# Performance work log

Measured on AMD Instinct MI355X. Metric: run time of the kernel, lower is better.

Reference implementation:

```python
import jax, jax.numpy as jnp
import numpy as np

HEAD_DIM = 128
N_HEADS = 32
ROPE_DIM = 64
TOPK = 1024
B, S, HID, QLORA = 1, 2048, 4096, 1536
LN_EPS = 1e-5  # torch nn.LayerNorm default


def _hadamard_matrix(n):
    H = np.array([[1.0]], dtype=np.float32)
    while H.shape[0] < n:
        H = np.block([[H, H], [H, -H]])
    return jnp.asarray(H)

_H128 = _hadamard_matrix(HEAD_DIM)
_FWHT_SCALE = HEAD_DIM ** -0.5


def rotate_activation(x):
    # Fast Walsh-Hadamard transform == x @ H_sylvester, scaled by dim**-0.5
    return (x @ _H128) * _FWHT_SCALE


def rope_non_interleaved(x, cos, sin):
    # x: [..., rope_dim]; cos/sin: broadcastable [..., rope_dim/2]
    half = x.shape[-1] // 2
    x1, x2 = x[..., :half], x[..., half:]
    return jnp.concatenate([x1 * cos - x2 * sin, x1 * sin + x2 * cos], axis=-1)


def setup_inputs() -> dict:
    key = jax.random.key(0)
    ks = jax.random.split(key, 8)
    hidden_states = jax.random.normal(ks[0], (B, S, HID), jnp.float32)
    q_compressed = jax.random.normal(ks[1], (B, S, QLORA), jnp.float32)
    # rotary cos/sin for rope_dim=64 (standard concat layout)
    pos = jnp.arange(S, dtype=jnp.float32)
    inv_freq = 1.0 / (10000.0 ** (jnp.arange(0, ROPE_DIM, 2, dtype=jnp.float32) / ROPE_DIM))
    ang = pos[:, None] * inv_freq[None, :]  # [S, 32]
    cos = jnp.tile(jnp.cos(ang), (1, 2))[None]  # [1, S, 64]
    sin = jnp.tile(jnp.sin(ang), (1, 2))[None]
    # additive causal mask [B, S, S]
    causal = jnp.tril(jnp.ones((S, S), jnp.bool_))
    attention_mask = jnp.where(causal, 0.0, -1e9).astype(jnp.float32)[None]
    Wq_b = jax.random.normal(ks[2], (QLORA, N_HEADS * HEAD_DIM), jnp.float32) * (QLORA ** -0.5)
    Wk = jax.random.normal(ks[3], (HID, HEAD_DIM), jnp.float32) * (HID ** -0.5)
    k_gamma = jnp.ones((HEAD_DIM,), jnp.float32)
    k_beta = jnp.zeros((HEAD_DIM,), jnp.float32)
    Ww = jax.random.normal(ks[4], (HID, N_HEADS), jnp.float32) * (HID ** -0.5)
    return {"hidden_states": hidden_states, "q_compressed": q_compressed, "cos": cos,
            "sin": sin, "attention_mask": attention_mask, "Wq_b": Wq_b, "Wk": Wk,
            "k_gamma": k_gamma, "k_beta": k_beta, "Ww": Ww}


def reference(hidden_states, q_compressed, cos, sin, attention_mask, Wq_b, Wk, k_gamma, k_beta, Ww):
    b, s, _ = hidden_states.shape
    softmax_scale = HEAD_DIM ** -0.5
    # queries: [b, s, H, D]
    q = (q_compressed @ Wq_b).reshape(b, s, N_HEADS, HEAD_DIM)
    q_rope, q_nope = q[..., :ROPE_DIM], q[..., ROPE_DIM:]
    # keys: single shared head, LayerNorm(k)
    k = hidden_states @ Wk  # [b, s, D]
    mu = jnp.mean(k, axis=-1, keepdims=True)
    var = jnp.mean(jnp.square(k - mu), axis=-1, keepdims=True)
    k = (k - mu) * jax.lax.rsqrt(var + LN_EPS) * k_gamma + k_beta
    k_rope, k_nope = k[..., :ROPE_DIM], k[..., ROPE_DIM:]
    # non-interleaved RoPE (cos/sin truncated to half_dim=32)
    half = ROPE_DIM // 2
    c, sn = cos[..., :half], sin[..., :half]
    q_rope = rope_non_interleaved(q_rope, c[:, :, None, :], sn[:, :, None, :])
    k_rope = rope_non_interleaved(k_rope, c, sn)
    q = jnp.concatenate([q_rope, q_nope], axis=-1)
    k = jnp.concatenate([k_rope, k_nope], axis=-1)
    # Hadamard activation rotation
    q = rotate_activation(q)
    k = rotate_activation(k)
    # I_{t,s} = sum_h w_{t,h} * ReLU(q_{t,h} . k_s) * scale
    scores = jax.nn.relu(jnp.einsum('bthd,bsd->bths', q, k)) * softmax_scale
    weights = hidden_states @ Ww  # [b, t, H]
    index_scores = jnp.einsum('bths,bth->bts', scores, weights)
    index_scores = index_scores + attention_mask
    topk = min(TOPK, s)
    _, topk_indices = jax.lax.top_k(index_scores, topk)  # [b, s, topk]
    return topk_indices, index_scores
```

## Files before the change

kernel.cpp:

```cpp
#include <hip/hip_runtime.h>
#include <stdint.h>

#define S_LEN 2048
#define HID 4096
#define QLORA 1536
#define NH 32
#define HD 128
#define TOPK_N 1024
#define NEG_INF -1000000000.0f
#define INV_SQRT_HD 0.08838834764831844f

typedef __attribute__((ext_vector_type(8))) short short8;
typedef __attribute__((ext_vector_type(4))) short short4_;
typedef __attribute__((ext_vector_type(4))) float float4_;
typedef __attribute__((ext_vector_type(4))) unsigned uint4_;
typedef __attribute__((ext_vector_type(4))) int int4_;
typedef __attribute__((ext_vector_type(2))) int int2_;

__device__ __forceinline__ short f2bf(float x) {
  union { float f; unsigned u; } v; v.f = x;
  unsigned r = v.u + 0x7FFFu + ((v.u >> 16) & 1u);
  return (short)(r >> 16);
}

__device__ __forceinline__ unsigned f2ord(float x) {
  union { float f; unsigned u; } v; v.f = x;
  return v.u ^ (0x80000000u | (unsigned)((int)v.u >> 31));
}

__device__ __forceinline__ void gload_lds16(const void* g, void* l) {
  __builtin_amdgcn_global_load_lds((const __attribute__((address_space(1))) unsigned int*)g,
                                   (__attribute__((address_space(3))) unsigned int*)l, 16, 0, 0);
}

__global__ __launch_bounds__(256) void prep_kernel(
    const float* __restrict__ hidden, short* __restrict__ hidb,
    const float* __restrict__ qc, char* __restrict__ qc8,
    float* __restrict__ kacc,
    const float* __restrict__ wqb, char* __restrict__ wq8T,
    const float* __restrict__ wk, const float* __restrict__ ww,
    short* __restrict__ kwT) {
  __shared__ __align__(8) char stile[4352];
  int bid = blockIdx.x;
  const int tid = threadIdx.x;
  if (bid < 8192) {
    int i = bid * 256 + tid;
    float4 v = ((const float4*)hidden)[i];
    short4_ o;
    o[0] = f2bf(v.x); o[1] = f2bf(v.y); o[2] = f2bf(v.z); o[3] = f2bf(v.w);
    ((short4_*)hidb)[i] = o;
    return;
  }
  if (bid < 9728) {
    int i = (bid - 8192) * 256 + tid;
    float4 f0 = ((const float4*)qc)[i * 2];
    float4 f1 = ((const float4*)qc)[i * 2 + 1];
    int lo = 0, hi = 0;
    lo = __builtin_amdgcn_cvt_pk_fp8_f32(f0.x, f0.y, lo, 0);
    lo = __builtin_amdgcn_cvt_pk_fp8_f32(f0.z, f0.w, lo, 1);
    hi = __builtin_amdgcn_cvt_pk_fp8_f32(f1.x, f1.y, hi, 0);
    hi = __builtin_amdgcn_cvt_pk_fp8_f32(f1.z, f1.w, hi, 1);
    ((int2_*)qc8)[i] = (int2_){lo, hi};
    return;
  }
  if (bid < 10048) {
    int i = (bid - 9728) * 256 + tid;
    ((float4_*)kacc)[i] = (float4_){0.f, 0.f, 0.f, 0.f};
    return;
  }
  if (bid < 13120) {
    char (*t8)[33] = (char(*)[33])stile;
    int b = bid - 10048;
    int k0 = (b >> 7) * 64, n0 = (b & 127) * 32;
    #pragma unroll
    for (int i = 0; i < 8; i++) {
      int e = tid + i * 256;
      int r = e >> 5, c = e & 31;
      float x = wqb[(size_t)(k0 + r) * HID + n0 + c];
      t8[r][c] = (char)__builtin_amdgcn_cvt_pk_fp8_f32(x, x, 0, 0);
    }
    __syncthreads();
    int nl = tid >> 3, jk = (tid & 7) * 8;
    union { char c[8]; long l; } o;
    #pragma unroll
    for (int j = 0; j < 8; j++) o.c[j] = t8[jk + j][nl];
    *(long*)(wq8T + (size_t)(n0 + nl) * QLORA + k0 + jk) = o.l;
    return;
  }
  short (*tile)[33] = (short(*)[33])stile;
  const float* in; short* out; int R, C, bx, by;
  if (bid < 13632) {
    int b2 = bid - 13120;
    in = wk; out = kwT; R = HID; C = HD; bx = b2 & 3; by = b2 >> 2;
  } else {
    int b3 = bid - 13632;
    in = ww; out = kwT + 128 * HID; R = HID; C = NH; bx = 0; by = b3;
  }
  int c0 = bx * 32, r0 = by * 32;
  int tx = tid & 31, ty = tid >> 5;
  #pragma unroll
  for (int i = 0; i < 32; i += 8)
    tile[ty + i][tx] = f2bf(in[(size_t)(r0 + ty + i) * C + c0 + tx]);
  __syncthreads();
  #pragma unroll
  for (int i = 0; i < 32; i += 8)
    out[(size_t)(c0 + ty + i) * R + r0 + tx] = tile[tx][ty + i];
}

#define QSTAGE8(kt, Ad, Bd) do { \
  _Pragma("unroll") \
  for (int i = 0; i < 4; i++) { \
    int m = w * 32 + i * 8 + lr; \
    int gb = (kt) * 128 + ((lc ^ (m & 7)) << 4); \
    gload_lds16(qc8 + (size_t)(t0 + m) * QLORA + gb, (Ad) + (w * 32 + i * 8) * 128); \
    gload_lds16(wq8T + (size_t)(n0 + m) * QLORA + gb, (Bd) + (w * 32 + i * 8) * 128); \
  } \
} while (0)

#define QCOMPUTE8(Aq, Bq) do { \
  _Pragma("unroll") \
  for (int p = 0; p < 4; p++) { \
    int ch = p * 2 + (quad >> 1); \
    int lo8 = (quad & 1) * 8; \
    long a[2], b[8]; \
    _Pragma("unroll") \
    for (int mt = 0; mt < 2; mt++) { \
      int m = w * 32 + mt * 16 + l15; \
      a[mt] = *(const long*)((Aq) + m * 128 + ((ch ^ (m & 7)) << 4) + lo8); \
    } \
    _Pragma("unroll") \
    for (int nt = 0; nt < 8; nt++) { \
      int n = nt * 16 + l15; \
      b[nt] = *(const long*)((Bq) + n * 128 + ((ch ^ (n & 7)) << 4) + lo8); \
    } \
    _Pragma("unroll") \
    for (int mt = 0; mt < 2; mt++) \
      _Pragma("unroll") \
      for (int nt = 0; nt < 8; nt++) \
        acc[mt][nt] = __builtin_amdgcn_mfma_f32_16x16x32_fp8_fp8(a[mt], b[nt], acc[mt][nt], 0, 0, 0); \
  } \
} while (0)

__global__ __launch_bounds__(256, 4) void gemms_kernel(
    const char* __restrict__ qc8, const char* __restrict__ wq8T,
    const float* __restrict__ cosp, const float* __restrict__ sinp,
    short* __restrict__ qrot,
    const short* __restrict__ hidb, const short* __restrict__ kwT,
    float* __restrict__ kacc) {
  __shared__ __align__(16) char smem[32768];
  const int tid = threadIdx.x;
  const int w = tid >> 6, lane = tid & 63;
  const int l15 = lane & 15, quad = lane >> 4;
  const int lr = lane >> 3, lc = lane & 7;

  if (blockIdx.x < 512) {
    char* A0 = smem;
    char* B0 = smem + 16384;
    const int n0 = (blockIdx.x & 31) * 128;
    const int t0 = (blockIdx.x >> 5) * 128;

    float4_ acc[2][8];
    #pragma unroll
    for (int mt = 0; mt < 2; mt++)
      #pragma unroll
      for (int i = 0; i < 8; i++) acc[mt][i] = (float4_){0.f, 0.f, 0.f, 0.f};

    QSTAGE8(0, A0, B0);
    __syncthreads();
    for (int kt = 0; ; kt++) {
      QCOMPUTE8(A0, B0);
      if (kt == 11) break;
      __syncthreads();
      QSTAGE8(kt + 1, A0, B0);
      __syncthreads();
    }

    #pragma unroll
    for (int mt = 0; mt < 2; mt++) {
      #pragma unroll
      for (int r = 0; r < 4; r++) {
        const int trow = t0 + w * 32 + mt * 16 + quad * 4 + r;
        float v[8];
        #pragma unroll
        for (int nt = 0; nt < 8; nt++) v[nt] = acc[mt][nt][r];
        float cc0 = cosp[trow * 64 + l15], cc1 = cosp[trow * 64 + 16 + l15];
        float ss0 = sinp[trow * 64 + l15], ss1 = sinp[trow * 64 + 16 + l15];
        float r0 = v[0] * cc0 - v[2] * ss0, r1 = v[1] * cc1 - v[3] * ss1;
        float r2 = v[0] * ss0 + v[2] * cc0, r3 = v[1] * ss1 + v[3] * cc1;
        v[0] = r0; v[1] = r1; v[2] = r2; v[3] = r3;
        short* orow = qrot + (size_t)trow * HID + n0;
        #pragma unroll
        for (int nt = 0; nt < 8; nt++)
          orow[nt * 16 + l15] = f2bf(v[nt]);
      }
    }
  } else {
    short* Al = (short*)smem;
    short* Bl = (short*)(smem + 8192);
    const int b2 = blockIdx.x - 512;
    const int kc0 = (b2 & 7) * 512;
    const int m0g = (b2 >> 3) * 64;

    float4_ acc[10];
    #pragma unroll
    for (int i = 0; i < 10; i++) acc[i] = (float4_){0.f, 0.f, 0.f, 0.f};

    for (int k0 = kc0; k0 < kc0 + 512; k0 += 64) {
      #pragma unroll
      for (int i = 0; i < 2; i++) {
        int m = w * 16 + i * 8 + lr;
        int gk = k0 + ((lc ^ (m & 7)) << 3);
        gload_lds16(hidb + (size_t)(m0g + m) * HID + gk, Al + (w * 16 + i * 8) * 64);
      }
      #pragma unroll
      for (int i = 0; i < 5; i++) {
        int n = w * 40 + i * 8 + lr;
        int gk = k0 + ((lc ^ (n & 7)) << 3);
        gload_lds16(kwT + (size_t)n * HID + gk, Bl + (w * 40 + i * 8) * 64);
      }
      __syncthreads();
      #pragma unroll
      for (int kk = 0; kk < 64; kk += 32) {
        int ca = (kk >> 3) + quad;
        int ma = w * 16 + l15;
        short8 a = *(const short8*)(Al + ma * 64 + ((ca ^ (ma & 7)) << 3));
        #pragma unroll
        for (int nt = 0; nt < 10; nt++) {
          int n = nt * 16 + l15;
          short8 b = *(const short8*)(Bl + n * 64 + ((ca ^ (n & 7)) << 3));
          acc[nt] = __builtin_amdgcn_mfma_f32_16x16x32_bf16(a, b, acc[nt], 0, 0, 0);
        }
      }
      __syncthreads();
    }
    #pragma unroll
    for (int nt = 0; nt < 10; nt++)
      #pragma unroll
      for (int r = 0; r < 4; r++) {
        int row = m0g + w * 16 + quad * 4 + r;
        atomicAdd(&kacc[(size_t)row * 160 + nt * 16 + l15], acc[nt][r]);
      }
  }
}

__global__ __launch_bounds__(256) void ln_rope_kernel(
    const float* __restrict__ kacc, const float* __restrict__ gamma,
    const float* __restrict__ beta, const float* __restrict__ cosp,
    const float* __restrict__ sinp, short* __restrict__ krot) {
  const int tid = threadIdx.x;
  const int row = blockIdx.x * 16 + (tid >> 4);
  const int l16 = tid & 15;
  const int c0 = l16 * 8;
  const float* rp = kacc + (size_t)row * 160 + c0;
  float4 f0 = ((const float4*)rp)[0], f1 = ((const float4*)rp)[1];
  float v[8] = {f0.x, f0.y, f0.z, f0.w, f1.x, f1.y, f1.z, f1.w};
  float s = 0.f, ss = 0.f;
  #pragma unroll
  for (int j = 0; j < 8; j++) { s += v[j]; ss += v[j] * v[j]; }
  #pragma unroll
  for (int d = 1; d <= 8; d <<= 1) {
    s += __shfl_xor(s, d, 64); ss += __shfl_xor(ss, d, 64);
  }
  float mu = s * (1.0f / 128.0f);
  float var = ss * (1.0f / 128.0f) - mu * mu;
  float rs = rsqrtf(var + 1e-5f);
  #pragma unroll
  for (int j = 0; j < 8; j++)
    v[j] = (v[j] - mu) * rs * gamma[c0 + j] + beta[c0 + j];
  #pragma unroll
  for (int j = 0; j < 8; j++) {
    float p = __shfl_xor(v[j], 4, 64);
    if (l16 < 8) {
      int idx = (c0 + j) & 31;
      float c = cosp[row * 64 + idx], sn = sinp[row * 64 + idx];
      v[j] = v[j] * c + p * ((l16 < 4) ? -sn : sn);
    }
  }
  short8 o;
  #pragma unroll
  for (int j = 0; j < 8; j++) o[j] = f2bf(v[j]);
  *(short8*)(krot + (size_t)row * 128 + c0) = o;
}

__global__ __launch_bounds__(256, 4) void scores_kernel(
    const short* __restrict__ qrot, const short* __restrict__ krot,
    const float* __restrict__ kacc, float* __restrict__ isc) {
  __shared__ __align__(16) char smem[32768];
  short* buf0 = (short*)smem;
  short* buf1 = (short*)(smem + 16384);

  const int tid = threadIdx.x;
  const int w = tid >> 6, lane = tid & 63;
  const int l15 = lane & 15, quad = lane >> 4;
  const int wm = w >> 1, wn = w & 1;
  const int lr16 = lane >> 4, lc16 = lane & 15;

  const int bid = blockIdx.x;
  const int strip = (bid & 1) ? (1023 - (bid >> 1)) : (bid >> 1);
  const int t0 = strip * 2;
  const int nch = (t0 + 1) / 64 + 1;

  const short* Abase = qrot + (size_t)t0 * 32 * 128;
  #pragma unroll
  for (int i = 0; i < 4; i++) {
    int m = (w * 4 + i) * 4 + lr16;
    int gofs = m * 128 + ((lc16 ^ (m & 7)) << 3);
    gload_lds16(Abase + gofs, buf1 + (w * 4 + i) * 512);
    gload_lds16(krot + gofs, buf0 + (w * 4 + i) * 512);
  }
  __syncthreads();

  short8 af[4][2];
  #pragma unroll
  for (int k4 = 0; k4 < 4; k4++) {
    int ca = k4 * 4 + quad;
    #pragma unroll
    for (int mt = 0; mt < 2; mt++) {
      int m = wm * 32 + mt * 16 + l15;
      af[k4][mt] = *(const short8*)(buf1 + m * 128 + ((ca ^ (m & 7)) << 3));
    }
  }
  const int trow = t0 + wm;
  float wq[2][4];
  #pragma unroll
  for (int mt = 0; mt < 2; mt++)
    #pragma unroll
    for (int r = 0; r < 4; r++)
      wq[mt][r] = kacc[(size_t)trow * 160 + 128 + mt * 16 + quad * 4 + r];
  __syncthreads();

  int cur = 0;
  for (int c = 0; c < nch; c++) {
    short* bcur = cur ? buf1 : buf0;
    if (c + 1 < nch) {
      short* bnxt = cur ? buf0 : buf1;
      const short* Bbase = krot + (size_t)(c + 1) * 64 * 128;
      #pragma unroll
      for (int i = 0; i < 4; i++) {
        int m = (w * 4 + i) * 4 + lr16;
        int gofs = m * 128 + ((lc16 ^ (m & 7)) << 3);
        gload_lds16(Bbase + gofs, bnxt + (w * 4 + i) * 512);
      }
    }

    float4_ acc[2][2];
    #pragma unroll
    for (int mt = 0; mt < 2; mt++)
      #pragma unroll
      for (int nt = 0; nt < 2; nt++) acc[mt][nt] = (float4_){0.f, 0.f, 0.f, 0.f};

    #pragma unroll
    for (int k4 = 0; k4 < 4; k4++) {
      int ca = k4 * 4 + quad;
      short8 b[2];
      #pragma unroll
      for (int nt = 0; nt < 2; nt++) {
        int n = wn * 32 + nt * 16 + l15;
        b[nt] = *(const short8*)(bcur + n * 128 + ((ca ^ (n & 7)) << 3));
      }
      #pragma unroll
      for (int mt = 0; mt < 2; mt++)
        #pragma unroll
        for (int nt = 0; nt < 2; nt++)
          acc[mt][nt] = __builtin_amdgcn_mfma_f32_16x16x32_bf16(af[k4][mt], b[nt], acc[mt][nt], 0, 0, 0);
    }

    #pragma unroll
    for (int nt = 0; nt < 2; nt++) {
      float p = 0.f;
      #pragma unroll
      for (int r = 0; r < 4; r++)
        p += fmaxf(acc[0][nt][r], 0.f) * wq[0][r] + fmaxf(acc[1][nt][r], 0.f) * wq[1][r];
      p += __shfl_xor(p, 16, 64); p += __shfl_xor(p, 32, 64);
      int s = c * 64 + wn * 32 + nt * 16 + l15;
      if (quad == 0)
        isc[(size_t)trow * S_LEN + s] = (s <= trow) ? p * INV_SQRT_HD : NEG_INF;
    }

    __syncthreads();
    cur ^= 1;
  }

  if (w < 2) {
    float4_ nf = (float4_){NEG_INF, NEG_INF, NEG_INF, NEG_INF};
    float4_* rowp = (float4_*)(isc + (size_t)(t0 + w) * S_LEN);
    for (int i = nch * 16 + lane; i < 512; i += 64) rowp[i] = nf;
  }
}


__device__ __forceinline__ void ce(unsigned &a, unsigned &b, bool d) {
  unsigned mx = a > b ? a : b;
  unsigned mn = a > b ? b : a;
  a = d ? mx : mn;
  b = d ? mn : mx;
}

__device__ __forceinline__ void mtop3(unsigned* v, bool d) {
  #pragma unroll
  for (int j = 16; j >= 4; j >>= 1)
    #pragma unroll
    for (int r = 0; r < 32; ++r)
      if (!(r & j)) ce(v[r], v[r ^ j], d);
}

template <int JT>
__device__ __forceinline__ void mreg(unsigned* v, bool d) {
  #pragma unroll
  for (int j = JT; j >= 1; j >>= 1)
    #pragma unroll
    for (int r = 0; r < 32; ++r)
      if (!(r & j)) ce(v[r], v[r ^ j], d);
}

#define IDX_L0   ((l << 5) | (q << 2))
#define IDX_654  (((l >> 2) << 7) | (q << 4) | ((l & 3) << 2))
#define IDX_765  (((l >> 3) << 8) | (q << 5) | ((l & 7) << 2))
#define IDX_876  (((l >> 4) << 9) | (q << 6) | ((l & 15) << 2))
#define IDX_543  (((l >> 1) << 6) | (q << 3) | ((l & 1) << 2))
#define IDX_987  (((l >> 5) << 10) | (q << 7) | ((l & 31) << 2))
#define IDX_1098 ((q << 8) | (l << 2))
#define SWZW(ix) ((ix) ^ ((((ix) >> 5) & 7) << 2))

#define RT(FROM, TO) do {                                               \
  _Pragma("unroll")                                                     \
  for (int q = 0; q < 8; ++q) {                                         \
    int ix = (FROM);                                                    \
    *(uint4_*)(buf + SWZW(ix)) =                                        \
        (uint4_){v[4 * q], v[4 * q + 1], v[4 * q + 2], v[4 * q + 3]};   \
  }                                                                     \
  _Pragma("unroll")                                                     \
  for (int q = 0; q < 8; ++q) {                                         \
    int ix = (TO);                                                      \
    uint4_ u = *(const uint4_*)(buf + SWZW(ix));                        \
    v[4 * q] = u[0]; v[4 * q + 1] = u[1];                               \
    v[4 * q + 2] = u[2]; v[4 * q + 3] = u[3];                           \
  }                                                                     \
} while (0)

__global__ __launch_bounds__(256) void topk_kernel(const float* __restrict__ isc,
                                                   int* __restrict__ idx_out) {
  __shared__ __align__(16) unsigned sbuf[4][2048];
  const int tid = threadIdx.x;
  const int w = tid >> 6, l = tid & 63;
  unsigned* buf = sbuf[w];
  const int gid = blockIdx.x * 4 + w;
  const bool shortrow = (gid < 512);
  int trow, sbase;
  if (shortrow) { trow = gid * 2 + (l >> 5); sbase = (l & 31) << 5; }
  else          { trow = 512 + gid;          sbase = l << 5; }

  unsigned v[32];
  {
    const float* rp = isc + (size_t)trow * S_LEN + sbase;
    #pragma unroll
    for (int g = 0; g < 8; ++g) {
      float4 f = ((const float4*)rp)[g];
      unsigned b0 = (unsigned)(2047 - (sbase + g * 4));
      v[g * 4 + 0] = (f2ord(f.x) & 0xFFFFF800u) | b0;
      v[g * 4 + 1] = (f2ord(f.y) & 0xFFFFF800u) | (b0 - 1);
      v[g * 4 + 2] = (f2ord(f.z) & 0xFFFFF800u) | (b0 - 2);
      v[g * 4 + 3] = (f2ord(f.w) & 0xFFFFF800u) | (b0 - 3);
    }
  }

  #pragma unroll
  for (int r = 0; r < 32; r += 2) ce(v[r], v[r + 1], ((r & 2) == 0));
  #pragma unroll
  for (int j = 2; j >= 1; j >>= 1)
    #pragma unroll
    for (int r = 0; r < 32; ++r)
      if (!(r & j)) ce(v[r], v[r ^ j], ((r & 4) == 0));
  #pragma unroll
  for (int j = 4; j >= 1; j >>= 1)
    #pragma unroll
    for (int r = 0; r < 32; ++r)
      if (!(r & j)) ce(v[r], v[r ^ j], ((r & 8) == 0));
  #pragma unroll
  for (int j = 8; j >= 1; j >>= 1)
    #pragma unroll
    for (int r = 0; r < 32; ++r)
      if (!(r & j)) ce(v[r], v[r ^ j], ((r & 16) == 0));

  mreg<16>(v, (l & 1) == 0);

  {
    bool d = ((l & 2) == 0);
    bool keep = (((l & 1) == 0) == d);
    #pragma unroll
    for (int r = 0; r < 32; ++r) {
      unsigned pv = (unsigned)__shfl_xor((int)v[r], 1, 64);
      unsigned mx = v[r] > pv ? v[r] : pv;
      unsigned mn = v[r] > pv ? pv : v[r];
      v[r] = keep ? mx : mn;
    }
    mreg<16>(v, d);
  }

  {
    bool d = ((l & 4) == 0);
    RT(IDX_L0, IDX_654);  mtop3(v, d);
    RT(IDX_654, IDX_L0);  mreg<8>(v, d);
  }
  {
    bool d = ((l & 8) == 0);
    RT(IDX_L0, IDX_765);  mtop3(v, d);
    RT(IDX_765, IDX_L0);  mreg<16>(v, d);
  }
  {
    bool d = ((l & 16) == 0);
    RT(IDX_L0, IDX_876);  mtop3(v, d);
    RT(IDX_876, IDX_543); mtop3(v, d);
    RT(IDX_543, IDX_L0);  mreg<4>(v, d);
  }
  {
    bool d = shortrow ? true : (l < 32);
    RT(IDX_L0, IDX_987);  mtop3(v, d);
    RT(IDX_987, IDX_654); mtop3(v, d);
    RT(IDX_654, IDX_L0);  mreg<8>(v, d);
  }
  if (!shortrow) {
    RT(IDX_L0, IDX_1098); mtop3(v, true);
    RT(IDX_1098, IDX_765); mtop3(v, true);
    RT(IDX_765, IDX_L0);  mreg<16>(v, true);
  }

  if (shortrow || l < 32) {
    int* op = idx_out + (size_t)trow * TOPK_N + sbase;
    #pragma unroll
    for (int g = 0; g < 8; ++g) {
      int4_ o;
      #pragma unroll
      for (int j = 0; j < 4; ++j) o[j] = 2047 - (int)(v[g * 4 + j] & 0x7FFu);
      ((int4_*)op)[g] = o;
    }
  }
}

extern "C" void kernel_launch(void* const* d_in, const int* in_sizes, int n_in,
                              void* d_out, int out_size, void* d_ws, size_t ws_size,
                              hipStream_t stream) {
  const float* hidden = (const float*)d_in[0];
  const float* qc     = (const float*)d_in[1];
  const float* cosp   = (const float*)d_in[2];
  const float* sinp   = (const float*)d_in[3];
  const float* wqb    = (const float*)d_in[5];
  const float* wk     = (const float*)d_in[6];
  const float* gamma  = (const float*)d_in[7];
  const float* beta   = (const float*)d_in[8];
  const float* ww     = (const float*)d_in[9];

  char* ws = (char*)d_ws;
  short* hidb = (short*)ws;
  char*  qc8  = (char*)(ws + 16777216);
  char*  wq8T = (char*)(ws + 19922944);
  short* kwT  = (short*)(ws + 26214400);
  short* krot = (short*)(ws + 27525120);
  short* qrot = (short*)(ws + 28049408);
  float* kacc = (float*)(ws + 44826624);

  int*   idx_out = (int*)d_out;
  float* isc     = ((float*)d_out) + (size_t)S_LEN * TOPK_N;

  prep_kernel<<<dim3(13760), dim3(256), 0, stream>>>(hidden, hidb, qc, qc8, kacc,
                                                     wqb, wq8T, wk, ww, kwT);
  gemms_kernel<<<dim3(768), dim3(256), 0, stream>>>(qc8, wq8T, cosp, sinp, qrot,
                                                    hidb, kwT, kacc);
  ln_rope_kernel<<<dim3(128), dim3(256), 0, stream>>>(kacc, gamma, beta, cosp, sinp, krot);
  scores_kernel<<<dim3(1024), dim3(256), 0, stream>>>(qrot, krot, kacc, isc);
  topk_kernel<<<dim3(384), dim3(256), 0, stream>>>(isc, idx_out);
}
```

Measured before the change: 226.3 us.

## Restructure scores kernel to one row per block with direct global register loads

The scores kernel now processes one query row per block over 2048 blocks instead of two rows per block, with each of four waves covering 16 keys per 64-key chunk. LDS staging and block barriers are dropped: A and B fragments are loaded straight from global memory into registers, with a two-chunk software double buffer in registers. This cuts synchronisation and LDS traffic and gives finer load balance across the causal triangle. In exchange each key row is fetched once per query row rather than being shared between two rows, so L2 traffic rises and the loads are uncoalesced.

New measurement: 259.6 us. 1.15x slower.

```diff
diff --git a/kernel.cpp b/kernel.cpp
--- a/kernel.cpp
+++ b/kernel.cpp
@@ -282,110 +282,70 @@
   *(short8*)(krot + (size_t)row * 128 + c0) = o;
 }
 
+#define SLOADB(bf, c) do {                                                     \
+  const short* Bb = krot + (size_t)((c) * 64 + w * 16 + l15) * 128 + quad * 8; \
+  bf[0] = *(const short8*)(Bb);                                                \
+  bf[1] = *(const short8*)(Bb + 32);                                           \
+  bf[2] = *(const short8*)(Bb + 64);                                           \
+  bf[3] = *(const short8*)(Bb + 96);                                           \
+} while (0)
+
+#define SCSTORE(bf, c) do {                                                    \
+  float4_ a0 = (float4_){0.f, 0.f, 0.f, 0.f};                                  \
+  float4_ a1 = (float4_){0.f, 0.f, 0.f, 0.f};                                  \
+  _Pragma("unroll")                                                            \
+  for (int k4 = 0; k4 < 4; k4++) {                                             \
+    a0 = __builtin_amdgcn_mfma_f32_16x16x32_bf16(af[k4][0], bf[k4], a0, 0, 0, 0); \
+    a1 = __builtin_amdgcn_mfma_f32_16x16x32_bf16(af[k4][1], bf[k4], a1, 0, 0, 0); \
+  }                                                                            \
+  float p = 0.f;                                                               \
+  _Pragma("unroll")                                                            \
+  for (int r = 0; r < 4; r++)                                                  \
+    p += fmaxf(a0[r], 0.f) * wq[0][r] + fmaxf(a1[r], 0.f) * wq[1][r];          \
+  p += __shfl_xor(p, 16, 64); p += __shfl_xor(p, 32, 64);                      \
+  int s = (c) * 64 + w * 16 + l15;                                             \
+  if (quad == 0)                                                               \
+    isc[(size_t)trow * S_LEN + s] = (s <= trow) ? p * INV_SQRT_HD : NEG_INF;   \
+} while (0)
+
 __global__ __launch_bounds__(256, 4) void scores_kernel(
     const short* __restrict__ qrot, const short* __restrict__ krot,
     const float* __restrict__ kacc, float* __restrict__ isc) {
-  __shared__ __align__(16) char smem[32768];
-  short* buf0 = (short*)smem;
-  short* buf1 = (short*)(smem + 16384);
-
   const int tid = threadIdx.x;
   const int w = tid >> 6, lane = tid & 63;
   const int l15 = lane & 15, quad = lane >> 4;
-  const int wm = w >> 1, wn = w & 1;
-  const int lr16 = lane >> 4, lc16 = lane & 15;
-
-  const int bid = blockIdx.x;
-  const int strip = (bid & 1) ? (1023 - (bid >> 1)) : (bid >> 1);
-  const int t0 = strip * 2;
-  const int nch = (t0 + 1) / 64 + 1;
-
-  const short* Abase = qrot + (size_t)t0 * 32 * 128;
-  #pragma unroll
-  for (int i = 0; i < 4; i++) {
-    int m = (w * 4 + i) * 4 + lr16;
-    int gofs = m * 128 + ((lc16 ^ (m & 7)) << 3);
-    gload_lds16(Abase + gofs, buf1 + (w * 4 + i) * 512);
-    gload_lds16(krot + gofs, buf0 + (w * 4 + i) * 512);
-  }
-  __syncthreads();
+
+  const int trow = 2047 - blockIdx.x;
+  const int nch = (trow + 64) >> 6;
 
   short8 af[4][2];
-  #pragma unroll
-  for (int k4 = 0; k4 < 4; k4++) {
-    int ca = k4 * 4 + quad;
-    #pragma unroll
-    for (int mt = 0; mt < 2; mt++) {
-      int m = wm * 32 + mt * 16 + l15;
-      af[k4][mt] = *(const short8*)(buf1 + m * 128 + ((ca ^ (m & 7)) << 3));
-    }
-  }
-  const int trow = t0 + wm;
+  const short* Ab = qrot + (size_t)trow * HID + quad * 8;
+  #pragma unroll
+  for (int k4 = 0; k4 < 4; k4++)
+    #pragma unroll
+    for (int mt = 0; mt < 2; mt++)
+      af[k4][mt] = *(const short8*)(Ab + (mt * 16 + l15) * 128 + k4 * 32);
+
   float wq[2][4];
   #pragma unroll
   for (int mt = 0; mt < 2; mt++)
     #pragma unroll
     for (int r = 0; r < 4; r++)
       wq[mt][r] = kacc[(size_t)trow * 160 + 128 + mt * 16 + quad * 4 + r];
-  __syncthreads();
-
-  int cur = 0;
-  for (int c = 0; c < nch; c++) {
-    short* bcur = cur ? buf1 : buf0;
-    if (c + 1 < nch) {
-      short* bnxt = cur ? buf0 : buf1;
-      const short* Bbase = krot + (size_t)(c + 1) * 64 * 128;
-      #pragma unroll
-      for (int i = 0; i < 4; i++) {
-        int m = (w * 4 + i) * 4 + lr16;
-        int gofs = m * 128 + ((lc16 ^ (m & 7)) << 3);
-        gload_lds16(Bbase + gofs, bnxt + (w * 4 + i) * 512);
-      }
-    }
-
-    float4_ acc[2][2];
-    #pragma unroll
-    for (int mt = 0; mt < 2; mt++)
-      #pragma unroll
-      for (int nt = 0; nt < 2; nt++) acc[mt][nt] = (float4_){0.f, 0.f, 0.f, 0.f};
-
-    #pragma unroll
-    for (int k4 = 0; k4 < 4; k4++) {
-      int ca = k4 * 4 + quad;
-      short8 b[2];
-      #pragma unroll
-      for (int nt = 0; nt < 2; nt++) {
-        int n = wn * 32 + nt * 16 + l15;
-        b[nt] = *(const short8*)(bcur + n * 128 + ((ca ^ (n & 7)) << 3));
-      }
-      #pragma unroll
-      for (int mt = 0; mt < 2; mt++)
-        #pragma unroll
-        for (int nt = 0; nt < 2; nt++)
-          acc[mt][nt] = __builtin_amdgcn_mfma_f32_16x16x32_bf16(af[k4][mt], b[nt], acc[mt][nt], 0, 0, 0);
-    }
-
-    #pragma unroll
-    for (int nt = 0; nt < 2; nt++) {
-      float p = 0.f;
-      #pragma unroll
-      for (int r = 0; r < 4; r++)
-        p += fmaxf(acc[0][nt][r], 0.f) * wq[0][r] + fmaxf(acc[1][nt][r], 0.f) * wq[1][r];
-      p += __shfl_xor(p, 16, 64); p += __shfl_xor(p, 32, 64);
-      int s = c * 64 + wn * 32 + nt * 16 + l15;
-      if (quad == 0)
-        isc[(size_t)trow * S_LEN + s] = (s <= trow) ? p * INV_SQRT_HD : NEG_INF;
-    }
-
-    __syncthreads();
-    cur ^= 1;
-  }
-
-  if (w < 2) {
-    float4_ nf = (float4_){NEG_INF, NEG_INF, NEG_INF, NEG_INF};
-    float4_* rowp = (float4_*)(isc + (size_t)(t0 + w) * S_LEN);
-    for (int i = nch * 16 + lane; i < 512; i += 64) rowp[i] = nf;
-  }
+
+  short8 bA[4], bB[4];
+  SLOADB(bA, 0);
+  for (int c = 0; c < nch; c += 2) {
+    if (c + 1 < nch) SLOADB(bB, c + 1);
+    SCSTORE(bA, c);
+    if (c + 1 >= nch) break;
+    if (c + 2 < nch) SLOADB(bA, c + 2);
+    SCSTORE(bB, c + 1);
+  }
+
+  float4_ nf = (float4_){NEG_INF, NEG_INF, NEG_INF, NEG_INF};
+  float4_* rowp = (float4_*)(isc + (size_t)trow * S_LEN);
+  for (int i = nch * 16 + tid; i < 512; i += 256) rowp[i] = nf;
 }
 
 
@@ -567,6 +527,6 @@
   gemms_kernel<<<dim3(768), dim3(256), 0, stream>>>(qc8, wq8T, cosp, sinp, qrot,
                                                     hidb, kwT, kacc);
   ln_rope_kernel<<<dim3(128), dim3(256), 0, stream>>>(kacc, gamma, beta, cosp, sinp, krot);
-  scores_kernel<<<dim3(1024), dim3(256), 0, stream>>>(qrot, krot, kacc, isc);
+  scores_kernel<<<dim3(2048), dim3(256), 0, stream>>>(qrot, krot, kacc, isc);
   topk_kernel<<<dim3(384), dim3(256), 0, stream>>>(isc, idx_out);
 }
```

## Fuse scores and top-k into one kernel using LDS row buffer

Applied to the files above, without the earlier changes.

Merges the scores kernel and the bitonic top-k kernel. Each block now keeps its two score rows in shared memory and sorts them itself, so the top-k pass no longer reloads the rows from global memory and one launch is removed. The cost is more LDS per block (48KB), lower occupancy (launch bound 3), and only two of the four waves working during the sort. Short rows now go through the full 2048-element sort instead of the cheaper half-row path.

New measurement: 239.5 us. 1.06x slower.

```diff
diff --git a/kernel.cpp b/kernel.cpp
--- a/kernel.cpp
+++ b/kernel.cpp
@@ -282,113 +282,6 @@
   *(short8*)(krot + (size_t)row * 128 + c0) = o;
 }
 
-__global__ __launch_bounds__(256, 4) void scores_kernel(
-    const short* __restrict__ qrot, const short* __restrict__ krot,
-    const float* __restrict__ kacc, float* __restrict__ isc) {
-  __shared__ __align__(16) char smem[32768];
-  short* buf0 = (short*)smem;
-  short* buf1 = (short*)(smem + 16384);
-
-  const int tid = threadIdx.x;
-  const int w = tid >> 6, lane = tid & 63;
-  const int l15 = lane & 15, quad = lane >> 4;
-  const int wm = w >> 1, wn = w & 1;
-  const int lr16 = lane >> 4, lc16 = lane & 15;
-
-  const int bid = blockIdx.x;
-  const int strip = (bid & 1) ? (1023 - (bid >> 1)) : (bid >> 1);
-  const int t0 = strip * 2;
-  const int nch = (t0 + 1) / 64 + 1;
-
-  const short* Abase = qrot + (size_t)t0 * 32 * 128;
-  #pragma unroll
-  for (int i = 0; i < 4; i++) {
-    int m = (w * 4 + i) * 4 + lr16;
-    int gofs = m * 128 + ((lc16 ^ (m & 7)) << 3);
-    gload_lds16(Abase + gofs, buf1 + (w * 4 + i) * 512);
-    gload_lds16(krot + gofs, buf0 + (w * 4 + i) * 512);
-  }
-  __syncthreads();
-
-  short8 af[4][2];
-  #pragma unroll
-  for (int k4 = 0; k4 < 4; k4++) {
-    int ca = k4 * 4 + quad;
-    #pragma unroll
-    for (int mt = 0; mt < 2; mt++) {
-      int m = wm * 32 + mt * 16 + l15;
-      af[k4][mt] = *(const short8*)(buf1 + m * 128 + ((ca ^ (m & 7)) << 3));
-    }
-  }
-  const int trow = t0 + wm;
-  float wq[2][4];
-  #pragma unroll
-  for (int mt = 0; mt < 2; mt++)
-    #pragma unroll
-    for (int r = 0; r < 4; r++)
-      wq[mt][r] = kacc[(size_t)trow * 160 + 128 + mt * 16 + quad * 4 + r];
-  __syncthreads();
-
-  int cur = 0;
-  for (int c = 0; c < nch; c++) {
-    short* bcur = cur ? buf1 : buf0;
-    if (c + 1 < nch) {
-      short* bnxt = cur ? buf0 : buf1;
-      const short* Bbase = krot + (size_t)(c + 1) * 64 * 128;
-      #pragma unroll
-      for (int i = 0; i < 4; i++) {
-        int m = (w * 4 + i) * 4 + lr16;
-        int gofs = m * 128 + ((lc16 ^ (m & 7)) << 3);
-        gload_lds16(Bbase + gofs, bnxt + (w * 4 + i) * 512);
-      }
-    }
-
-    float4_ acc[2][2];
-    #pragma unroll
-    for (int mt = 0; mt < 2; mt++)
-      #pragma unroll
-      for (int nt = 0; nt < 2; nt++) acc[mt][nt] = (float4_){0.f, 0.f, 0.f, 0.f};
-
-    #pragma unroll
-    for (int k4 = 0; k4 < 4; k4++) {
-      int ca = k4 * 4 + quad;
-      short8 b[2];
-      #pragma unroll
-      for (int nt = 0; nt < 2; nt++) {
-        int n = wn * 32 + nt * 16 + l15;
-        b[nt] = *(const short8*)(bcur + n * 128 + ((ca ^ (n & 7)) << 3));
-      }
-      #pragma unroll
-      for (int mt = 0; mt < 2; mt++)
-        #pragma unroll
-        for (int nt = 0; nt < 2; nt++)
-          acc[mt][nt] = __builtin_amdgcn_mfma_f32_16x16x32_bf16(af[k4][mt], b[nt], acc[mt][nt], 0, 0, 0);
-    }
-
-    #pragma unroll
-    for (int nt = 0; nt < 2; nt++) {
-      float p = 0.f;
-      #pragma unroll
-      for (int r = 0; r < 4; r++)
-        p += fmaxf(acc[0][nt][r], 0.f) * wq[0][r] + fmaxf(acc[1][nt][r], 0.f) * wq[1][r];
-      p += __shfl_xor(p, 16, 64); p += __shfl_xor(p, 32, 64);
-      int s = c * 64 + wn * 32 + nt * 16 + l15;
-      if (quad == 0)
-        isc[(size_t)trow * S_LEN + s] = (s <= trow) ? p * INV_SQRT_HD : NEG_INF;
-    }
-
-    __syncthreads();
-    cur ^= 1;
-  }
-
-  if (w < 2) {
-    float4_ nf = (float4_){NEG_INF, NEG_INF, NEG_INF, NEG_INF};
-    float4_* rowp = (float4_*)(isc + (size_t)(t0 + w) * S_LEN);
-    for (int i = nch * 16 + lane; i < 512; i += 64) rowp[i] = nf;
-  }
-}
-
-
 __device__ __forceinline__ void ce(unsigned &a, unsigned &b, bool d) {
   unsigned mx = a > b ? a : b;
   unsigned mn = a > b ? b : a;
@@ -438,21 +331,127 @@
   }                                                                     \
 } while (0)
 
-__global__ __launch_bounds__(256) void topk_kernel(const float* __restrict__ isc,
-                                                   int* __restrict__ idx_out) {
-  __shared__ __align__(16) unsigned sbuf[4][2048];
+__global__ __launch_bounds__(256, 3) void scores_topk_kernel(
+    const short* __restrict__ qrot, const short* __restrict__ krot,
+    const float* __restrict__ kacc, float* __restrict__ isc,
+    int* __restrict__ idx_out) {
+  __shared__ __align__(16) char smem[49152];
+  short* buf0 = (short*)smem;
+  short* buf1 = (short*)(smem + 16384);
+  float (*rowbuf)[2048] = (float(*)[2048])(smem + 32768);
+
   const int tid = threadIdx.x;
-  const int w = tid >> 6, l = tid & 63;
-  unsigned* buf = sbuf[w];
-  const int gid = blockIdx.x * 4 + w;
-  const bool shortrow = (gid < 512);
-  int trow, sbase;
-  if (shortrow) { trow = gid * 2 + (l >> 5); sbase = (l & 31) << 5; }
-  else          { trow = 512 + gid;          sbase = l << 5; }
+  const int w = tid >> 6, lane = tid & 63;
+  const int l15 = lane & 15, quad = lane >> 4;
+  const int wm = w >> 1, wn = w & 1;
+  const int lr16 = lane >> 4, lc16 = lane & 15;
+
+  const int bid = blockIdx.x;
+  const int strip = (bid & 1) ? (1023 - (bid >> 1)) : (bid >> 1);
+  const int t0 = strip * 2;
+  const int nch = (t0 + 1) / 64 + 1;
+
+  const short* Abase = qrot + (size_t)t0 * 32 * 128;
+  #pragma unroll
+  for (int i = 0; i < 4; i++) {
+    int m = (w * 4 + i) * 4 + lr16;
+    int gofs = m * 128 + ((lc16 ^ (m & 7)) << 3);
+    gload_lds16(Abase + gofs, buf1 + (w * 4 + i) * 512);
+    gload_lds16(krot + gofs, buf0 + (w * 4 + i) * 512);
+  }
+  __syncthreads();
+
+  short8 af[4][2];
+  #pragma unroll
+  for (int k4 = 0; k4 < 4; k4++) {
+    int ca = k4 * 4 + quad;
+    #pragma unroll
+    for (int mt = 0; mt < 2; mt++) {
+      int m = wm * 32 + mt * 16 + l15;
+      af[k4][mt] = *(const short8*)(buf1 + m * 128 + ((ca ^ (m & 7)) << 3));
+    }
+  }
+  const int trow = t0 + wm;
+  float wq[2][4];
+  #pragma unroll
+  for (int mt = 0; mt < 2; mt++)
+    #pragma unroll
+    for (int r = 0; r < 4; r++)
+      wq[mt][r] = kacc[(size_t)trow * 160 + 128 + mt * 16 + quad * 4 + r];
+  __syncthreads();
+
+  int cur = 0;
+  for (int c = 0; c < nch; c++) {
+    short* bcur = cur ? buf1 : buf0;
+    if (c + 1 < nch) {
+      short* bnxt = cur ? buf0 : buf1;
+      const short* Bbase = krot + (size_t)(c + 1) * 64 * 128;
+      #pragma unroll
+      for (int i = 0; i < 4; i++) {
+        int m = (w * 4 + i) * 4 + lr16;
+        int gofs = m * 128 + ((lc16 ^ (m & 7)) << 3);
+        gload_lds16(Bbase + gofs, bnxt + (w * 4 + i) * 512);
+      }
+    }
+
+    float4_ acc[2][2];
+    #pragma unroll
+    for (int mt = 0; mt < 2; mt++)
+      #pragma unroll
+      for (int nt = 0; nt < 2; nt++) acc[mt][nt] = (float4_){0.f, 0.f, 0.f, 0.f};
+
+    #pragma unroll
+    for (int k4 = 0; k4 < 4; k4++) {
+      int ca = k4 * 4 + quad;
+      short8 b[2];
+      #pragma unroll
+      for (int nt = 0; nt < 2; nt++) {
+        int n = wn * 32 + nt * 16 + l15;
+        b[nt] = *(const short8*)(bcur + n * 128 + ((ca ^ (n & 7)) << 3));
+      }
+      #pragma unroll
+      for (int mt = 0; mt < 2; mt++)
+        #pragma unroll
+        for (int nt = 0; nt < 2; nt++)
+          acc[mt][nt] = __builtin_amdgcn_mfma_f32_16x16x32_bf16(af[k4][mt], b[nt], acc[mt][nt], 0, 0, 0);
+    }
+
+    #pragma unroll
+    for (int nt = 0; nt < 2; nt++) {
+      float p = 0.f;
+      #pragma unroll
+      for (int r = 0; r < 4; r++)
+        p += fmaxf(acc[0][nt][r], 0.f) * wq[0][r] + fmaxf(acc[1][nt][r], 0.f) * wq[1][r];
+      p += __shfl_xor(p, 16, 64); p += __shfl_xor(p, 32, 64);
+      int s = c * 64 + wn * 32 + nt * 16 + l15;
+      if (quad == 0) {
+        float val = (s <= trow) ? p * INV_SQRT_HD : NEG_INF;
+        isc[(size_t)trow * S_LEN + s] = val;
+        rowbuf[wm][s] = val;
+      }
+    }
+
+    __syncthreads();
+    cur ^= 1;
+  }
+
+  if (w < 2) {
+    float4_ nf = (float4_){NEG_INF, NEG_INF, NEG_INF, NEG_INF};
+    float4_* rowp = (float4_*)(isc + (size_t)(t0 + w) * S_LEN);
+    float4_* rowl = (float4_*)rowbuf[w];
+    for (int i = nch * 16 + lane; i < 512; i += 64) { rowp[i] = nf; rowl[i] = nf; }
+  }
+  __syncthreads();
+
+  if (w >= 2) return;
+  const int l = lane;
+  unsigned* buf = (unsigned*)rowbuf[w];
+  const int srow = t0 + w;
+  const int sbase = l << 5;
 
   unsigned v[32];
   {
-    const float* rp = isc + (size_t)trow * S_LEN + sbase;
+    const float* rp = rowbuf[w] + sbase;
     #pragma unroll
     for (int g = 0; g < 8; ++g) {
       float4 f = ((const float4*)rp)[g];
@@ -514,19 +513,19 @@
     RT(IDX_543, IDX_L0);  mreg<4>(v, d);
   }
   {
-    bool d = shortrow ? true : (l < 32);
+    bool d = (l < 32);
     RT(IDX_L0, IDX_987);  mtop3(v, d);
     RT(IDX_987, IDX_654); mtop3(v, d);
     RT(IDX_654, IDX_L0);  mreg<8>(v, d);
   }
-  if (!shortrow) {
+  {
     RT(IDX_L0, IDX_1098); mtop3(v, true);
     RT(IDX_1098, IDX_765); mtop3(v, true);
     RT(IDX_765, IDX_L0);  mreg<16>(v, true);
   }
 
-  if (shortrow || l < 32) {
-    int* op = idx_out + (size_t)trow * TOPK_N + sbase;
+  if (l < 32) {
+    int* op = idx_out + (size_t)srow * TOPK_N + sbase;
     #pragma unroll
     for (int g = 0; g < 8; ++g) {
       int4_ o;
@@ -567,6 +566,5 @@
   gemms_kernel<<<dim3(768), dim3(256), 0, stream>>>(qc8, wq8T, cosp, sinp, qrot,
                                                     hidb, kwT, kacc);
   ln_rope_kernel<<<dim3(128), dim3(256), 0, stream>>>(kacc, gamma, beta, cosp, sinp, krot);
-  scores_kernel<<<dim3(1024), dim3(256), 0, stream>>>(qrot, krot, kacc, isc);
-  topk_kernel<<<dim3(384), dim3(256), 0, stream>>>(isc, idx_out);
-}
+  scores_topk_kernel<<<dim3(1024), dim3(256), 0, stream>>>(qrot, krot, kacc, isc, idx_out);
+}
```
